# Performance work log

Hardware: AMD Instinct MI355X
Metric: run time of the kernel (lower is better)

## Reference

```python
import jax, jax.numpy as jnp
import numpy as np

NUM_HEADS = 16
LN_EPS = 1e-5


def pos_encoding(length, d):
    pos = jnp.arange(length, dtype=jnp.float32)[:, None]
    i = jnp.arange(d, dtype=jnp.float32)[None, :]
    angle = pos / jnp.power(10000.0, (2.0 * jnp.floor(i / 2.0)) / d)
    return jnp.where((jnp.arange(d) % 2) == 0, jnp.sin(angle), jnp.cos(angle))


def rel_shift(x):
    # x: (B, H, l, m) -> TXL shift trick
    b, h, l, m = x.shape
    x = jnp.concatenate([x, jnp.zeros((b, h, l, 1), x.dtype)], axis=-1)
    x = x.reshape(b, h, l * (m + 1))
    return x[:, :, l - 1:-1].reshape(b, h, l, m)


def layer_norm(x, g, b):
    mu = jnp.mean(x, axis=-1, keepdims=True)
    var = jnp.mean(jnp.square(x - mu), axis=-1, keepdims=True)
    return (x - mu) * jax.lax.rsqrt(var + LN_EPS) * g + b


def setup_inputs() -> dict:
    key = jax.random.key(0)
    B, S, M, D, L, V = 2, 1024, 1024, 1024, 4, 32000
    ks = jax.random.split(key, 32)
    s = 0.02
    d = {
        'inputs': jax.random.randint(ks[0], (B, S), 0, V, dtype=jnp.int32),
        'mems': jax.random.normal(ks[1], (L, B, M, D), jnp.float32),
        'emb': jax.random.normal(ks[2], (V, D), jnp.float32) * s,
        'Wq': jax.random.normal(ks[3], (L, D, D), jnp.float32) * s,
        'bq': jnp.zeros((L, D), jnp.float32),
        'Wke': jax.random.normal(ks[4], (L, D, D), jnp.float32) * s,
        'bke': jnp.zeros((L, D), jnp.float32),
        'Wkr': jax.random.normal(ks[5], (L, D, D), jnp.float32) * s,
        'bkr': jnp.zeros((L, D), jnp.float32),
        'Wv': jax.random.normal(ks[6], (L, D, D), jnp.float32) * s,
        'bv': jnp.zeros((L, D), jnp.float32),
        'Wo': jax.random.normal(ks[7], (L, D, D), jnp.float32) * s,
        'bo': jnp.zeros((L, D), jnp.float32),
        'ln1_g': jnp.ones((L, D), jnp.float32),
        'ln1_b': jnp.zeros((L, D), jnp.float32),
        'W1': jax.random.normal(ks[8], (L, D, D), jnp.float32) * s,
        'b1': jnp.zeros((L, D), jnp.float32),
        'W2': jax.random.normal(ks[9], (L, D, D), jnp.float32) * s,
        'b2': jnp.zeros((L, D), jnp.float32),
        'ln2_g': jnp.ones((L, D), jnp.float32),
        'ln2_b': jnp.zeros((L, D), jnp.float32),
        'Wh': jax.random.normal(ks[10], (D, D), jnp.float32) * s,
        'bh': jnp.zeros((D,), jnp.float32),
        'Wf': jax.random.normal(ks[11], (D, V), jnp.float32) * s,
        'bf': jnp.zeros((V,), jnp.float32),
        'next_mem_len': 1024,
    }
    return d


def reference(inputs, mems, emb, Wq, bq, Wke, bke, Wkr, bkr, Wv, bv, Wo, bo,
              ln1_g, ln1_b, W1, b1, W2, b2, ln2_g, ln2_b, Wh, bh, Wf, bf,
              next_mem_len):
    B, S = inputs.shape
    L, _, M, D = mems.shape
    T = M + S
    H = NUM_HEADS
    dh = D // H
    sqrt_dk = jnp.sqrt(jnp.float32(dh))

    rel_enc = pos_encoding(T, D)[::-1]  # (T, D), reversed
    # look-ahead mask: query i may attend key j iff j <= i + M
    mask = (jnp.arange(T)[None, :] > (jnp.arange(S)[:, None] + M)).astype(jnp.float32)
    mask = mask[None, None] * -1e9  # (1,1,S,T)

    x = emb[inputs] * jnp.sqrt(jnp.float32(D))  # (B,S,D)

    for l in range(L):
        x_tilde = jnp.concatenate([mems[l], x], axis=1)  # (B,T,D)
        q = (x @ Wq[l] + bq[l]).reshape(B, S, H, dh).transpose(0, 2, 1, 3)
        k = (x_tilde @ Wke[l] + bke[l]).reshape(B, T, H, dh).transpose(0, 2, 1, 3)
        v = (x_tilde @ Wv[l] + bv[l]).reshape(B, T, H, dh).transpose(0, 2, 1, 3)
        A = jnp.einsum('bhsd,bhtd->bhst', q, k)
        Qr = (rel_enc @ Wkr[l] + bkr[l]).reshape(T, H, dh).transpose(1, 0, 2)  # (H,T,dh)
        B_hat = jnp.einsum('bhsd,htd->bhst', q, Qr)
        score = (A + rel_shift(B_hat)) / sqrt_dk + mask
        attn = jax.nn.softmax(score, axis=-1)
        ctx = jnp.einsum('bhst,bhtd->bhsd', attn, v)
        ctx = ctx.transpose(0, 2, 1, 3).reshape(B, S, D)
        attn_out = ctx @ Wo[l] + bo[l]
        h1 = layer_norm(x + attn_out, ln1_g[l], ln1_b[l])
        ff = jax.nn.gelu(h1 @ W1[l] + b1[l], approximate=False) @ W2[l] + b2[l]
        x = layer_norm(h1 + ff, ln2_g[l], ln2_b[l])

    x = jax.nn.gelu(x @ Wh + bh, approximate=False)
    logits = x @ Wf + bf
    return logits
```

## Files before the change

kernel.cpp:

```cpp
#include <hip/hip_runtime.h>
#include <hip/hip_bf16.h>
#include <math.h>

typedef __attribute__((ext_vector_type(4))) float f32x4;
typedef __attribute__((ext_vector_type(8))) short s16x8;

#define BB 2
#define SS 1024
#define MEM 1024
#define DD 1024
#define LL 4
#define VV 32000
#define TT 2048
#define NH 16
#define DH 64

__device__ __forceinline__ short f2bf(float f) {
    unsigned u = __float_as_uint(f);
    u += 0x7fffu + ((u >> 16) & 1u);
    return (short)(u >> 16);
}

__device__ __forceinline__ float gelu_f(float x) {
    return 0.5f * x * (1.0f + erff(x * 0.70710678118654752f));
}

__device__ __forceinline__ void gll16(const short* g, short* l) {
    __builtin_amdgcn_global_load_lds(
        (__attribute__((address_space(1))) void*)(short*)g,
        (__attribute__((address_space(3))) void*)l, 16, 0, 0);
}

template<int WM, int WN>
__global__ __launch_bounds__(256) void gemm_bf16(
    const short* __restrict__ A, const short* __restrict__ Bt,
    const float* __restrict__ bias, const float* __restrict__ bias2,
    int nsplit, void* __restrict__ Cv, int N, int K, int nby, int act, int obf)
{
    constexpr int BM = WM * 32, BN = WN * 32;
    constexpr int NA = BM / 32, NB = BN / 32;
    __shared__ short a_s[BM * 64];
    __shared__ short b_s[BN * 64];
    const int tid  = threadIdx.x;
    const int lane = tid & 63;
    const int wave = tid >> 6;
    const int wr = wave >> 1, wc = wave & 1;
    const int fr = lane & 15, fg = lane >> 4;

    const int nwg = gridDim.x;
    const int bid = blockIdx.x;
    const int swz = ((nwg & 7) == 0) ? ((bid & 7) * (nwg >> 3) + (bid >> 3)) : bid;
    const size_t m0 = (size_t)(swz % nby) * BM;
    const size_t n0 = (size_t)(swz / nby) * BN;

    const short* gA[NA]; short* lA[NA];
    const short* gB[NB]; short* lB[NB];
    #pragma unroll
    for (int i = 0; i < NA; ++i) {
        const int s   = i * 256 + tid;
        const int row = (s >> 7) * 16 + (s & 15);
        const int kof = ((s >> 4) & 7) * 8;
        gA[i] = A + (m0 + row) * (size_t)K + kof;
        lA[i] = &a_s[s * 8];
    }
    #pragma unroll
    for (int i = 0; i < NB; ++i) {
        const int s   = i * 256 + tid;
        const int nn  = (s >> 7) * 16 + (s & 15);
        const int kof = ((s >> 4) & 7) * 8;
        gB[i] = Bt + (n0 + nn) * (size_t)K + kof;
        lB[i] = &b_s[s * 8];
    }

    f32x4 acc[WM][WN] = {};

    #pragma unroll
    for (int i = 0; i < NA; ++i) gll16(gA[i], lA[i]);
    #pragma unroll
    for (int i = 0; i < NB; ++i) gll16(gB[i], lB[i]);

    const int nt = K >> 6;
    for (int t = 0; t < nt; ++t) {
        __syncthreads();
        s16x8 af[WM][2], bf[WN][2];
        #pragma unroll
        for (int mi = 0; mi < WM; ++mi)
            #pragma unroll
            for (int h = 0; h < 2; ++h)
                af[mi][h] = *(const s16x8*)&a_s[((wr*WM + mi)*128 + (h*4 + fg)*16 + fr) * 8];
        #pragma unroll
        for (int ni = 0; ni < WN; ++ni)
            #pragma unroll
            for (int h = 0; h < 2; ++h)
                bf[ni][h] = *(const s16x8*)&b_s[((wc*WN + ni)*128 + (h*4 + fg)*16 + fr) * 8];
        if (t + 1 < nt) {
            __syncthreads();
            const int koff = (t + 1) << 6;
            #pragma unroll
            for (int i = 0; i < NA; ++i) gll16(gA[i] + koff, lA[i]);
            #pragma unroll
            for (int i = 0; i < NB; ++i) gll16(gB[i] + koff, lB[i]);
        }
        #pragma unroll
        for (int mi = 0; mi < WM; ++mi)
            #pragma unroll
            for (int ni = 0; ni < WN; ++ni) {
                acc[mi][ni] = __builtin_amdgcn_mfma_f32_16x16x32_bf16(
                    af[mi][0], bf[ni][0], acc[mi][ni], 0, 0, 0);
                acc[mi][ni] = __builtin_amdgcn_mfma_f32_16x16x32_bf16(
                    af[mi][1], bf[ni][1], acc[mi][ni], 0, 0, 0);
            }
    }

    float* Cf = (float*)Cv;
    short* Cb = (short*)Cv;
    #pragma unroll
    for (int mi = 0; mi < WM; ++mi) {
        #pragma unroll
        for (int ni = 0; ni < WN; ++ni) {
            const size_t r0 = m0 + wr*WM*16 + mi*16 + fg*4;
            const size_t c  = n0 + wc*WN*16 + ni*16 + fr;
            const float bb = (c < (size_t)nsplit) ? bias[c] : bias2[c - nsplit];
            #pragma unroll
            for (int rg = 0; rg < 4; ++rg) {
                float vv = acc[mi][ni][rg] + bb;
                if (act) vv = gelu_f(vv);
                if (obf) Cb[(r0 + rg)*(size_t)N + c] = f2bf(vv);
                else     Cf[(r0 + rg)*(size_t)N + c] = vv;
            }
        }
    }
}

__global__ __launch_bounds__(256) void transpose7_kernel(
    const float* w0, const float* w1, const float* w2, const float* w3,
    const float* w4, const float* w5, const float* w6, short* out)
{
    __shared__ float t[32][33];
    const int z = blockIdx.z;
    const float* W;
    switch (z) {
        case 0: W = w0; break; case 1: W = w1; break; case 2: W = w2; break;
        case 3: W = w3; break; case 4: W = w4; break; case 5: W = w5; break;
        default: W = w6; break;
    }
    short* O = out + (size_t)z * DD * DD;
    const int tid = threadIdx.x;
    const int k0 = blockIdx.y * 32, n0 = blockIdx.x * 32;
    const int r = tid >> 3, c4 = (tid & 7) * 4;
    float4 v = *(const float4*)&W[(size_t)(k0 + r) * DD + n0 + c4];
    t[r][c4+0] = v.x; t[r][c4+1] = v.y; t[r][c4+2] = v.z; t[r][c4+3] = v.w;
    __syncthreads();
    short4 o;
    o.x = f2bf(t[c4+0][r]); o.y = f2bf(t[c4+1][r]);
    o.z = f2bf(t[c4+2][r]); o.w = f2bf(t[c4+3][r]);
    *(short4*)&O[(size_t)(n0 + r) * DD + k0 + c4] = o;
}

__global__ __launch_bounds__(256) void transposeF_kernel(
    const float* __restrict__ W, short* __restrict__ O)
{
    __shared__ float t[32][33];
    const int tid = threadIdx.x;
    const int k0 = blockIdx.y * 32, n0 = blockIdx.x * 32;
    const int r = tid >> 3, c4 = (tid & 7) * 4;
    float4 v = *(const float4*)&W[(size_t)(k0 + r) * VV + n0 + c4];
    t[r][c4+0] = v.x; t[r][c4+1] = v.y; t[r][c4+2] = v.z; t[r][c4+3] = v.w;
    __syncthreads();
    short4 o;
    o.x = f2bf(t[c4+0][r]); o.y = f2bf(t[c4+1][r]);
    o.z = f2bf(t[c4+2][r]); o.w = f2bf(t[c4+3][r]);
    *(short4*)&O[(size_t)(n0 + r) * DD + k0 + c4] = o;
}

__global__ __launch_bounds__(256) void attn_kernel(
    const short* __restrict__ q, const short* __restrict__ k,
    const short* __restrict__ v, const short* __restrict__ Qr,
    short* __restrict__ ctx, int kstr, int qstr)
{
    __shared__ short k_s[32][72];
    __shared__ short qr_s[96][72];
    __shared__ short vT_s[64][40];
    __shared__ float a_t[64][33];
    __shared__ float b_ts[64][33];
    __shared__ short p_s[64][40];
    __shared__ float row_m[64], row_l[64], row_sc[64];

    const int tid  = threadIdx.x;
    const int id   = blockIdx.x;
    const int bh   = id & 31;
    const int qi   = ((id >> 5) + bh) & 15;
    const int q0   = qi * 64;
    const int b    = bh >> 4;
    const int h    = bh & 15;
    const int hoff = h * DH;

    const int lane = tid & 63;
    const int wave = tid >> 6;
    const int fr   = lane & 15;
    const int fg   = lane >> 4;
    const int tk  = tid >> 3, ck = (tid & 7) * 8;
    const int iq  = tid >> 2, cq = (tid & 3) * 16;
    const int iq2 = 64 + (tid >> 3), cq2 = (tid & 7) * 8;
    const int sr  = tid >> 2, sc0 = (tid & 3) * 8;

    const short* qrow = q + ((size_t)(b * SS + q0 + 16 * wave + fr)) * DD + hoff;
    s16x8 aq0 = *(const s16x8*)(qrow + fg * 8);
    s16x8 aq1 = *(const s16x8*)(qrow + 32 + fg * 8);

    if (tid < 64) { row_m[tid] = -INFINITY; row_l[tid] = 0.0f; }

    const int t_end = q0 + 64 + MEM;
    const int u0b   = SS - 1 - (q0 + 63);

    s16x8 kf, vf, rA, rB, rC;
    auto loadT = [&](int t0) {
        kf = *(const s16x8*)(k + ((size_t)(b * TT + t0 + tk)) * kstr + hoff + ck);
        vf = *(const s16x8*)(v + ((size_t)(b * TT + t0 + tk)) * kstr + hoff + ck);
        int u1 = t0 + u0b + iq;
        u1 = u1 < 0 ? 0 : (u1 > TT - 1 ? TT - 1 : u1);
        const short* rp = Qr + (size_t)u1 * qstr + hoff + cq;
        rA = *(const s16x8*)rp;
        rB = *(const s16x8*)(rp + 8);
        int u2 = t0 + u0b + iq2;
        u2 = u2 < 0 ? 0 : (u2 > TT - 1 ? TT - 1 : u2);
        rC = *(const s16x8*)(Qr + (size_t)u2 * qstr + hoff + cq2);
    };
    loadT(0);

    f32x4 opv[4] = {};
    const int nlo = 3 - wave, nhi = 5 - wave;

    for (int t0 = 0; t0 < t_end; t0 += 32) {
        __syncthreads();
        {
            *(s16x8*)&k_s[tk][ck] = kf;
            const int tsw = tk ^ (((ck >> 3) & 3) << 3);
            vT_s[ck + 0][tsw] = vf[0];
            vT_s[ck + 1][tsw] = vf[1];
            vT_s[ck + 2][tsw] = vf[2];
            vT_s[ck + 3][tsw] = vf[3];
            vT_s[ck + 4][tsw] = vf[4];
            vT_s[ck + 5][tsw] = vf[5];
            vT_s[ck + 6][tsw] = vf[6];
            vT_s[ck + 7][tsw] = vf[7];
            *(s16x8*)&qr_s[iq][cq]      = rA;
            *(s16x8*)&qr_s[iq][cq + 8]  = rB;
            *(s16x8*)&qr_s[iq2][cq2]    = rC;
        }
        if (t0 + 32 < t_end) loadT(t0 + 32);
        __syncthreads();

        {
            #pragma unroll
            for (int n = 0; n < 2; ++n) {
                s16x8 b0 = *(const s16x8*)&k_s[16*n + fr][fg * 8];
                s16x8 b1 = *(const s16x8*)&k_s[16*n + fr][32 + fg * 8];
                f32x4 ca = {0, 0, 0, 0};
                ca = __builtin_amdgcn_mfma_f32_16x16x32_bf16(aq0, b0, ca, 0, 0, 0);
                ca = __builtin_amdgcn_mfma_f32_16x16x32_bf16(aq1, b1, ca, 0, 0, 0);
                #pragma unroll
                for (int rg = 0; rg < 4; ++rg)
                    a_t[16*wave + 4*fg + rg][16*n + fr] = ca[rg];
            }
        }
        {
            #pragma unroll
            for (int n = 0; n < 6; ++n) {
                if (n < nlo || n > nhi) continue;
                s16x8 c0 = *(const s16x8*)&qr_s[16*n + fr][fg * 8];
                s16x8 c1 = *(const s16x8*)&qr_s[16*n + fr][32 + fg * 8];
                f32x4 cb = {0, 0, 0, 0};
                cb = __builtin_amdgcn_mfma_f32_16x16x32_bf16(aq0, c0, cb, 0, 0, 0);
                cb = __builtin_amdgcn_mfma_f32_16x16x32_bf16(aq1, c1, cb, 0, 0, 0);
                #pragma unroll
                for (int rg = 0; rg < 4; ++rg) {
                    const int r  = 16*wave + 4*fg + rg;
                    const int tl = 16*n + fr - 63 + r;
                    if ((unsigned)tl < 32u) b_ts[r][tl] = cb[rg];
                }
            }
        }
        __syncthreads();

        {
            const int sg = q0 + sr;
            float sv[8];
            #pragma unroll
            for (int j = 0; j < 8; ++j) {
                const int c = sc0 + j;
                float x = (a_t[sr][c] + b_ts[sr][c]) * 0.125f;
                sv[j] = (t0 + c > sg + MEM) ? -1e30f : x;
            }
            float mx = sv[0];
            #pragma unroll
            for (int j = 1; j < 8; ++j) mx = fmaxf(mx, sv[j]);
            mx = fmaxf(mx, __shfl_xor(mx, 1, 64));
            mx = fmaxf(mx, __shfl_xor(mx, 2, 64));
            const float mo = row_m[sr];
            const float mn = fmaxf(mo, mx);
            const float scl = __expf(mo - mn);
            float sum = 0.0f;
            s16x8 pp;
            #pragma unroll
            for (int j = 0; j < 8; ++j) {
                float e = __expf(sv[j] - mn);
                sum += e;
                pp[j] = f2bf(e);
            }
            sum += __shfl_xor(sum, 1, 64);
            sum += __shfl_xor(sum, 2, 64);
            if ((tid & 3) == 0) {
                row_m[sr]  = mn;
                row_sc[sr] = scl;
                row_l[sr]  = row_l[sr] * scl + sum;
            }
            *(s16x8*)&p_s[sr][sc0] = pp;
        }
        __syncthreads();

        {
            f32x4 scv;
            #pragma unroll
            for (int rg = 0; rg < 4; ++rg) scv[rg] = row_sc[16*wave + 4*fg + rg];
            #pragma unroll
            for (int n = 0; n < 4; ++n)
                #pragma unroll
                for (int rg = 0; rg < 4; ++rg) opv[n][rg] *= scv[rg];
            s16x8 ap = *(const s16x8*)&p_s[16*wave + fr][fg * 8];
            #pragma unroll
            for (int n = 0; n < 4; ++n) {
                const int d = 16*n + fr;
                s16x8 bv = *(const s16x8*)&vT_s[d][(fg ^ ((d >> 3) & 3)) * 8];
                opv[n] = __builtin_amdgcn_mfma_f32_16x16x32_bf16(ap, bv, opv[n], 0, 0, 0);
            }
        }
    }

    {
        #pragma unroll
        for (int rg = 0; rg < 4; ++rg) {
            const int r = 16*wave + 4*fg + rg;
            const float inv = 1.0f / row_l[r];
            short* op = ctx + ((size_t)(b * SS + q0 + r)) * DD + hoff;
            #pragma unroll
            for (int n = 0; n < 4; ++n)
                op[16*n + fr] = f2bf(opv[n][rg] * inv);
        }
    }
}

__global__ __launch_bounds__(256) void addln_kernel(
    const float* __restrict__ a, const float* __restrict__ b,
    const float* __restrict__ g, const float* __restrict__ be,
    float* __restrict__ out32, short* __restrict__ outbf)
{
    __shared__ float red[8];
    const int row = blockIdx.x;
    const int tid = threadIdx.x;
    const size_t base = (size_t)row * DD;
    const int c = tid * 4;
    float4 xa = *(const float4*)(a + base + c);
    float4 xb = *(const float4*)(b + base + c);
    float x0 = xa.x + xb.x, x1 = xa.y + xb.y, x2 = xa.z + xb.z, x3 = xa.w + xb.w;
    float s  = x0 + x1 + x2 + x3;
    float sq = x0 * x0 + x1 * x1 + x2 * x2 + x3 * x3;
    #pragma unroll
    for (int o = 32; o > 0; o >>= 1) {
        s  += __shfl_down(s, o, 64);
        sq += __shfl_down(sq, o, 64);
    }
    const int wv = tid >> 6;
    if ((tid & 63) == 0) { red[wv * 2] = s; red[wv * 2 + 1] = sq; }
    __syncthreads();
    float ts = red[0] + red[2] + red[4] + red[6];
    float tq = red[1] + red[3] + red[5] + red[7];
    float mu  = ts * (1.0f / DD);
    float var = tq * (1.0f / DD) - mu * mu;
    float rs  = rsqrtf(var + 1e-5f);
    float4 gv = *(const float4*)(g + c);
    float4 bv = *(const float4*)(be + c);
    float4 o4;
    o4.x = (x0 - mu) * rs * gv.x + bv.x;
    o4.y = (x1 - mu) * rs * gv.y + bv.y;
    o4.z = (x2 - mu) * rs * gv.z + bv.z;
    o4.w = (x3 - mu) * rs * gv.w + bv.w;
    *(float4*)(out32 + base + c) = o4;
    short4 ob;
    ob.x = f2bf(o4.x); ob.y = f2bf(o4.y); ob.z = f2bf(o4.z); ob.w = f2bf(o4.w);
    *(short4*)(outbf + base + c) = ob;
}

__global__ __launch_bounds__(256) void embed_kernel(
    const int* __restrict__ inp, const float* __restrict__ emb,
    float* __restrict__ x32, short* __restrict__ xbf)
{
    const int row = blockIdx.x;
    const int c = threadIdx.x * 4;
    const int idx = inp[row];
    float4 vv = *(const float4*)(emb + (size_t)idx * DD + c);
    vv.x *= 32.0f; vv.y *= 32.0f; vv.z *= 32.0f; vv.w *= 32.0f;
    *(float4*)(x32 + (size_t)row * DD + c) = vv;
    short4 ob;
    ob.x = f2bf(vv.x); ob.y = f2bf(vv.y); ob.z = f2bf(vv.z); ob.w = f2bf(vv.w);
    *(short4*)(xbf + (size_t)row * DD + c) = ob;
}

__global__ __launch_bounds__(256) void concat_kernel(
    const float* __restrict__ mems_l, const short* __restrict__ xbf,
    short* __restrict__ xt)
{
    size_t i = ((size_t)blockIdx.x * 256 + threadIdx.x) * 8;
    size_t bt = i / DD;
    int d = (int)(i - bt * DD);
    int b = (int)(bt / TT);
    int t = (int)(bt - (size_t)b * TT);
    s16x8 o;
    if (t < MEM) {
        const float* mp = mems_l + ((size_t)(b * MEM + t)) * DD + d;
        float4 a0 = *(const float4*)mp;
        float4 a1 = *(const float4*)(mp + 4);
        o[0] = f2bf(a0.x); o[1] = f2bf(a0.y); o[2] = f2bf(a0.z); o[3] = f2bf(a0.w);
        o[4] = f2bf(a1.x); o[5] = f2bf(a1.y); o[6] = f2bf(a1.z); o[7] = f2bf(a1.w);
    } else {
        o = *(const s16x8*)(xbf + ((size_t)(b * SS + (t - MEM))) * DD + d);
    }
    *(s16x8*)(xt + i) = o;
}

__global__ __launch_bounds__(256) void relenc_kernel(short* __restrict__ re)
{
    const int u = blockIdx.x;
    const int p = TT - 1 - u;
    const int i0 = threadIdx.x * 4;
    short4 o;
    #pragma unroll
    for (int j = 0; j < 4; ++j) {
        int i = i0 + j;
        float ex   = (float)(2 * (i >> 1)) * (1.0f / DD);
        float invf = __expf(-ex * 9.210340371976184f);
        float ang  = (float)p * invf;
        float val  = (i & 1) ? cosf(ang) : sinf(ang);
        ((short*)&o)[j] = f2bf(val);
    }
    *(short4*)&re[(size_t)u * DD + i0] = o;
}

extern "C" void kernel_launch(void* const* d_in, const int* in_sizes, int n_in,
                              void* d_out, int out_size, void* d_ws, size_t ws_size,
                              hipStream_t stream)
{
    const int*   inp  = (const int*)d_in[0];
    const float* mems = (const float*)d_in[1];
    const float* emb  = (const float*)d_in[2];
    const float* Wq   = (const float*)d_in[3];
    const float* bq   = (const float*)d_in[4];
    const float* Wke  = (const float*)d_in[5];
    const float* bke  = (const float*)d_in[6];
    const float* Wkr  = (const float*)d_in[7];
    const float* bkr  = (const float*)d_in[8];
    const float* Wv   = (const float*)d_in[9];
    const float* bv   = (const float*)d_in[10];
    const float* Wo   = (const float*)d_in[11];
    const float* bo   = (const float*)d_in[12];
    const float* ln1g = (const float*)d_in[13];
    const float* ln1b = (const float*)d_in[14];
    const float* W1   = (const float*)d_in[15];
    const float* b1   = (const float*)d_in[16];
    const float* W2   = (const float*)d_in[17];
    const float* b2   = (const float*)d_in[18];
    const float* ln2g = (const float*)d_in[19];
    const float* ln2b = (const float*)d_in[20];
    const float* Wh   = (const float*)d_in[21];
    const float* bh   = (const float*)d_in[22];
    const float* Wf   = (const float*)d_in[23];
    const float* bfb  = (const float*)d_in[24];

    char* wsb = (char*)d_ws;
    size_t off = 0;
    auto alloc = [&](size_t bytes) { char* p = wsb + off; off += (bytes + 255) & ~(size_t)255; return p; };
    float* h132  = (float*)alloc((size_t)BB*SS*DD*4);
    float* ao32  = (float*)alloc((size_t)BB*SS*DD*4);
    float* ff232 = (float*)alloc((size_t)BB*SS*DD*4);
    short* xt    = (short*)alloc((size_t)BB*TT*DD*2);
    short* qb    = (short*)alloc((size_t)BB*SS*DD*2);
    short* kvb   = (short*)alloc((size_t)BB*TT*DD*2*2);
    short* ctxb  = (short*)alloc((size_t)BB*SS*DD*2);
    short* ff1   = (short*)alloc((size_t)BB*SS*DD*2);
    float* x32   = (float*)alloc((size_t)BB*SS*DD*4);
    short* x_bf  = (short*)alloc((size_t)BB*SS*DD*2);
    short* whout = (short*)alloc((size_t)BB*SS*DD*2);
    short* rel   = (short*)alloc((size_t)TT*DD*2);
    short* qr4   = (short*)alloc((size_t)SS*2*4*DD*2);
    short* wt6   = (short*)alloc((size_t)6*DD*DD*2);
    short* wkr4  = (short*)h132;
    short* wft   = (short*)h132;

    relenc_kernel<<<TT, 256, 0, stream>>>(rel);
    embed_kernel<<<BB * SS, 256, 0, stream>>>(inp, emb, x32, x_bf);

    const size_t WOFF = (size_t)DD * DD;

    transpose7_kernel<<<dim3(32, 32, 4), 256, 0, stream>>>(
        Wkr + 0*WOFF, Wkr + 1*WOFF, Wkr + 2*WOFF, Wkr + 3*WOFF, Wq, Wq, Wq, wkr4);
    gemm_bf16<4,4><<<dim3(512), 256, 0, stream>>>(
        rel, wkr4, bkr, bkr, 4*DD, qr4, 4*DD, DD, TT/128, 0, 1);

    const int gSm = (DD / 64) * ((BB * SS) / 64);
    const int gKV = ((2 * DD) / 128) * ((BB * TT) / 128);

    for (int l = 0; l < LL; ++l) {
        const size_t wo  = (size_t)l * DD * DD;
        const size_t bo_ = (size_t)l * DD;
        transpose7_kernel<<<dim3(32, 32, 6), 256, 0, stream>>>(
            Wq + wo, Wke + wo, Wv + wo, Wo + wo, W1 + wo, W2 + wo, Wq, wt6);
        concat_kernel<<<(BB * TT * DD / 8) / 256, 256, 0, stream>>>(
            mems + (size_t)l * BB * MEM * DD, x_bf, xt);
        gemm_bf16<2,2><<<dim3(gSm), 256, 0, stream>>>(
            x_bf, wt6 + 0*WOFF, bq + bo_, bq + bo_, DD, qb, DD, DD, (BB*SS)/64, 0, 1);
        gemm_bf16<4,4><<<dim3(gKV), 256, 0, stream>>>(
            xt, wt6 + 1*WOFF, bke + bo_, bv + bo_, DD, kvb, 2*DD, DD, (BB*TT)/128, 0, 1);
        attn_kernel<<<dim3((SS / 64) * BB * NH), 256, 0, stream>>>(
            qb, kvb, kvb + DD, qr4 + (size_t)l * DD, ctxb, 2 * DD, 4 * DD);
        gemm_bf16<2,2><<<dim3(gSm), 256, 0, stream>>>(
            ctxb, wt6 + 3*WOFF, bo + bo_, bo + bo_, DD, ao32, DD, DD, (BB*SS)/64, 0, 0);
        addln_kernel<<<BB * SS, 256, 0, stream>>>(x32, ao32, ln1g + bo_, ln1b + bo_, h132, x_bf);
        gemm_bf16<2,2><<<dim3(gSm), 256, 0, stream>>>(
            x_bf, wt6 + 4*WOFF, b1 + bo_, b1 + bo_, DD, ff1, DD, DD, (BB*SS)/64, 1, 1);
        gemm_bf16<2,2><<<dim3(gSm), 256, 0, stream>>>(
            ff1, wt6 + 5*WOFF, b2 + bo_, b2 + bo_, DD, ff232, DD, DD, (BB*SS)/64, 0, 0);
        addln_kernel<<<BB * SS, 256, 0, stream>>>(h132, ff232, ln2g + bo_, ln2b + bo_, x32, x_bf);
    }

    transpose7_kernel<<<dim3(32, 32, 1), 256, 0, stream>>>(
        Wh, Wh, Wh, Wh, Wh, Wh, Wh, wt6);
    transposeF_kernel<<<dim3(VV / 32, DD / 32), 256, 0, stream>>>(Wf, wft);
    gemm_bf16<2,2><<<dim3(gSm), 256, 0, stream>>>(
        x_bf, wt6, bh, bh, DD, whout, DD, DD, (BB*SS)/64, 1, 1);
    gemm_bf16<4,4><<<dim3((VV / 128) * ((BB * SS) / 128)), 256, 0, stream>>>(
        whout, wft, bfb, bfb, VV, (float*)d_out, VV, DD, (BB*SS)/128, 0, 0);
}
```

Before: 1.415 ms.

## Triple-buffer GEMM K-loop and widen attention tile with wave-local softmax

The GEMM kernel moves from a single-buffer 64-wide K step to a three-stage LDS ring of 32-wide K slices. Global-to-LDS loads are issued two stages ahead and guarded by explicit vmcnt waits and raw barriers, which is meant to hide load latency. The attention kernel doubles its key tile to 64 and accumulates the relative-position term directly into the score buffer, dropping one LDS array. Softmax running max and sum move into registers and are shared with shuffles, removing two block-wide barriers per tile. In exchange, LDS use and register pressure go up, and the correctness of the manual waitcnt and barrier ordering becomes harder to verify.

```diff
diff --git a/kernel.cpp b/kernel.cpp
--- a/kernel.cpp
+++ b/kernel.cpp
@@ -31,6 +31,15 @@
         (__attribute__((address_space(3))) void*)l, 16, 0, 0);
 }
 
+template<int N> __device__ __forceinline__ void vm_wait() {
+    if constexpr (N == 0)      asm volatile("s_waitcnt vmcnt(0)" ::: "memory");
+    else if constexpr (N == 2) asm volatile("s_waitcnt vmcnt(2)" ::: "memory");
+    else if constexpr (N == 3) asm volatile("s_waitcnt vmcnt(3)" ::: "memory");
+    else if constexpr (N == 4) asm volatile("s_waitcnt vmcnt(4)" ::: "memory");
+    else if constexpr (N == 6) asm volatile("s_waitcnt vmcnt(6)" ::: "memory");
+    else                       asm volatile("s_waitcnt vmcnt(8)" ::: "memory");
+}
+
 template<int WM, int WN>
 __global__ __launch_bounds__(256) void gemm_bf16(
     const short* __restrict__ A, const short* __restrict__ Bt,
@@ -38,9 +47,11 @@
     int nsplit, void* __restrict__ Cv, int N, int K, int nby, int act, int obf)
 {
     constexpr int BM = WM * 32, BN = WN * 32;
-    constexpr int NA = BM / 32, NB = BN / 32;
-    __shared__ short a_s[BM * 64];
-    __shared__ short b_s[BN * 64];
+    constexpr int NA = BM / 64, NB = BN / 64;
+    constexpr int L  = NA + NB;
+    constexpr int ASZ = BM * 32, BSZ = BN * 32;
+    __shared__ short a_s[3 * ASZ];
+    __shared__ short b_s[3 * BSZ];
     const int tid  = threadIdx.x;
     const int lane = tid & 63;
     const int wave = tid >> 6;
@@ -58,58 +69,58 @@
     #pragma unroll
     for (int i = 0; i < NA; ++i) {
         const int s   = i * 256 + tid;
-        const int row = (s >> 7) * 16 + (s & 15);
-        const int kof = ((s >> 4) & 7) * 8;
-        gA[i] = A + (m0 + row) * (size_t)K + kof;
+        const int row = (s >> 6) * 16 + (s & 15);
+        const int ks  = (s >> 4) & 3;
+        gA[i] = A + (m0 + row) * (size_t)K + ks * 8;
         lA[i] = &a_s[s * 8];
     }
     #pragma unroll
     for (int i = 0; i < NB; ++i) {
         const int s   = i * 256 + tid;
-        const int nn  = (s >> 7) * 16 + (s & 15);
-        const int kof = ((s >> 4) & 7) * 8;
-        gB[i] = Bt + (n0 + nn) * (size_t)K + kof;
+        const int nn  = (s >> 6) * 16 + (s & 15);
+        const int ks  = (s >> 4) & 3;
+        gB[i] = Bt + (n0 + nn) * (size_t)K + ks * 8;
         lB[i] = &b_s[s * 8];
     }
 
+    auto stage = [&](int t, int buf) {
+        const int koff = t << 5;
+        #pragma unroll
+        for (int i = 0; i < NA; ++i) gll16(gA[i] + koff, lA[i] + buf * ASZ);
+        #pragma unroll
+        for (int i = 0; i < NB; ++i) gll16(gB[i] + koff, lB[i] + buf * BSZ);
+    };
+
     f32x4 acc[WM][WN] = {};
 
-    #pragma unroll
-    for (int i = 0; i < NA; ++i) gll16(gA[i], lA[i]);
-    #pragma unroll
-    for (int i = 0; i < NB; ++i) gll16(gB[i], lB[i]);
-
-    const int nt = K >> 6;
+    const int nt = K >> 5;
+    stage(0, 0);
+    stage(1, 1);
+
+    int cur = 0;
     for (int t = 0; t < nt; ++t) {
-        __syncthreads();
-        s16x8 af[WM][2], bf[WN][2];
+        if (t + 1 < nt) vm_wait<L>();
+        else            vm_wait<0>();
+        __builtin_amdgcn_s_barrier();
+        __builtin_amdgcn_sched_barrier(0);
+        if (t + 2 < nt) stage(t + 2, cur == 0 ? 2 : cur - 1);
+
+        const short* ab = &a_s[cur * ASZ];
+        const short* bb = &b_s[cur * BSZ];
+        s16x8 af[WM], bf[WN];
         #pragma unroll
         for (int mi = 0; mi < WM; ++mi)
-            #pragma unroll
-            for (int h = 0; h < 2; ++h)
-                af[mi][h] = *(const s16x8*)&a_s[((wr*WM + mi)*128 + (h*4 + fg)*16 + fr) * 8];
+            af[mi] = *(const s16x8*)&ab[((wr*WM + mi)*64 + fg*16 + fr) * 8];
         #pragma unroll
         for (int ni = 0; ni < WN; ++ni)
-            #pragma unroll
-            for (int h = 0; h < 2; ++h)
-                bf[ni][h] = *(const s16x8*)&b_s[((wc*WN + ni)*128 + (h*4 + fg)*16 + fr) * 8];
-        if (t + 1 < nt) {
-            __syncthreads();
-            const int koff = (t + 1) << 6;
-            #pragma unroll
-            for (int i = 0; i < NA; ++i) gll16(gA[i] + koff, lA[i]);
-            #pragma unroll
-            for (int i = 0; i < NB; ++i) gll16(gB[i] + koff, lB[i]);
-        }
+            bf[ni] = *(const s16x8*)&bb[((wc*WN + ni)*64 + fg*16 + fr) * 8];
         #pragma unroll
         for (int mi = 0; mi < WM; ++mi)
             #pragma unroll
-            for (int ni = 0; ni < WN; ++ni) {
+            for (int ni = 0; ni < WN; ++ni)
                 acc[mi][ni] = __builtin_amdgcn_mfma_f32_16x16x32_bf16(
-                    af[mi][0], bf[ni][0], acc[mi][ni], 0, 0, 0);
-                acc[mi][ni] = __builtin_amdgcn_mfma_f32_16x16x32_bf16(
-                    af[mi][1], bf[ni][1], acc[mi][ni], 0, 0, 0);
-            }
+                    af[mi], bf[ni], acc[mi][ni], 0, 0, 0);
+        cur = (cur == 2) ? 0 : cur + 1;
     }
 
     float* Cf = (float*)Cv;
@@ -178,13 +189,11 @@
     const short* __restrict__ v, const short* __restrict__ Qr,
     short* __restrict__ ctx, int kstr, int qstr)
 {
-    __shared__ short k_s[32][72];
-    __shared__ short qr_s[96][72];
-    __shared__ short vT_s[64][40];
-    __shared__ float a_t[64][33];
-    __shared__ float b_ts[64][33];
-    __shared__ short p_s[64][40];
-    __shared__ float row_m[64], row_l[64], row_sc[64];
+    __shared__ short k_s[64][72];
+    __shared__ short vT_s[64][72];
+    __shared__ short qr_s[128][72];
+    __shared__ float a_t[64][67];
+    __shared__ short p_s[64][72];
 
     const int tid  = threadIdx.x;
     const int id   = blockIdx.x;
@@ -199,61 +208,63 @@
     const int wave = tid >> 6;
     const int fr   = lane & 15;
     const int fg   = lane >> 4;
-    const int tk  = tid >> 3, ck = (tid & 7) * 8;
-    const int iq  = tid >> 2, cq = (tid & 3) * 16;
-    const int iq2 = 64 + (tid >> 3), cq2 = (tid & 7) * 8;
-    const int sr  = tid >> 2, sc0 = (tid & 3) * 8;
+    const int tk = tid >> 2, ck = (tid & 3) * 16;
+    const int rq = tid >> 1, dq = (tid & 1) * 32;
+    const int sr  = tid >> 2;
+    const int sc0 = (tid & 3) * 16;
 
     const short* qrow = q + ((size_t)(b * SS + q0 + 16 * wave + fr)) * DD + hoff;
     s16x8 aq0 = *(const s16x8*)(qrow + fg * 8);
     s16x8 aq1 = *(const s16x8*)(qrow + 32 + fg * 8);
 
-    if (tid < 64) { row_m[tid] = -INFINITY; row_l[tid] = 0.0f; }
+    float m_r = -1e30f, l_r = 0.0f;
 
     const int t_end = q0 + 64 + MEM;
-    const int u0b   = SS - 1 - (q0 + 63);
-
-    s16x8 kf, vf, rA, rB, rC;
+    const int u0b   = SS - 1 - q0 - 63;
+
+    s16x8 kf0, kf1, vf0, vf1, rf0, rf1, rf2, rf3;
     auto loadT = [&](int t0) {
-        kf = *(const s16x8*)(k + ((size_t)(b * TT + t0 + tk)) * kstr + hoff + ck);
-        vf = *(const s16x8*)(v + ((size_t)(b * TT + t0 + tk)) * kstr + hoff + ck);
-        int u1 = t0 + u0b + iq;
-        u1 = u1 < 0 ? 0 : (u1 > TT - 1 ? TT - 1 : u1);
-        const short* rp = Qr + (size_t)u1 * qstr + hoff + cq;
-        rA = *(const s16x8*)rp;
-        rB = *(const s16x8*)(rp + 8);
-        int u2 = t0 + u0b + iq2;
-        u2 = u2 < 0 ? 0 : (u2 > TT - 1 ? TT - 1 : u2);
-        rC = *(const s16x8*)(Qr + (size_t)u2 * qstr + hoff + cq2);
+        const short* kp = k + ((size_t)(b * TT + t0 + tk)) * kstr + hoff + ck;
+        const short* vp = v + ((size_t)(b * TT + t0 + tk)) * kstr + hoff + ck;
+        kf0 = *(const s16x8*)kp;  kf1 = *(const s16x8*)(kp + 8);
+        vf0 = *(const s16x8*)vp;  vf1 = *(const s16x8*)(vp + 8);
+        int u = t0 + u0b + rq;
+        u = u < 0 ? 0 : (u > TT - 1 ? TT - 1 : u);
+        const short* rp = Qr + (size_t)u * qstr + hoff + dq;
+        rf0 = *(const s16x8*)rp;        rf1 = *(const s16x8*)(rp + 8);
+        rf2 = *(const s16x8*)(rp + 16); rf3 = *(const s16x8*)(rp + 24);
     };
     loadT(0);
 
     f32x4 opv[4] = {};
-    const int nlo = 3 - wave, nhi = 5 - wave;
-
-    for (int t0 = 0; t0 < t_end; t0 += 32) {
-        __syncthreads();
+    const int nlo = 3 - wave, nhi = 7 - wave;
+
+    for (int t0 = 0; t0 < t_end; t0 += 64) {
+        asm volatile("" ::: "memory");
+        __builtin_amdgcn_s_barrier();
+        __builtin_amdgcn_sched_barrier(0);
         {
-            *(s16x8*)&k_s[tk][ck] = kf;
-            const int tsw = tk ^ (((ck >> 3) & 3) << 3);
-            vT_s[ck + 0][tsw] = vf[0];
-            vT_s[ck + 1][tsw] = vf[1];
-            vT_s[ck + 2][tsw] = vf[2];
-            vT_s[ck + 3][tsw] = vf[3];
-            vT_s[ck + 4][tsw] = vf[4];
-            vT_s[ck + 5][tsw] = vf[5];
-            vT_s[ck + 6][tsw] = vf[6];
-            vT_s[ck + 7][tsw] = vf[7];
-            *(s16x8*)&qr_s[iq][cq]      = rA;
-            *(s16x8*)&qr_s[iq][cq + 8]  = rB;
-            *(s16x8*)&qr_s[iq2][cq2]    = rC;
+            *(s16x8*)&k_s[tk][ck]     = kf0;
+            *(s16x8*)&k_s[tk][ck + 8] = kf1;
+            #pragma unroll
+            for (int i = 0; i < 8; ++i) {
+                const int d0 = ck + i, d1 = ck + 8 + i;
+                vT_s[d0][tk ^ (((d0 >> 3) & 3) << 3)] = vf0[i];
+                vT_s[d1][tk ^ (((d1 >> 3) & 3) << 3)] = vf1[i];
+            }
+            *(s16x8*)&qr_s[rq][dq]      = rf0;
+            *(s16x8*)&qr_s[rq][dq + 8]  = rf1;
+            *(s16x8*)&qr_s[rq][dq + 16] = rf2;
+            *(s16x8*)&qr_s[rq][dq + 24] = rf3;
         }
-        if (t0 + 32 < t_end) loadT(t0 + 32);
-        __syncthreads();
+        if (t0 + 64 < t_end) loadT(t0 + 64);
+        asm volatile("s_waitcnt lgkmcnt(0)" ::: "memory");
+        __builtin_amdgcn_s_barrier();
+        __builtin_amdgcn_sched_barrier(0);
 
         {
             #pragma unroll
-            for (int n = 0; n < 2; ++n) {
+            for (int n = 0; n < 4; ++n) {
                 s16x8 b0 = *(const s16x8*)&k_s[16*n + fr][fg * 8];
                 s16x8 b1 = *(const s16x8*)&k_s[16*n + fr][32 + fg * 8];
                 f32x4 ca = {0, 0, 0, 0};
@@ -266,7 +277,7 @@
         }
         {
             #pragma unroll
-            for (int n = 0; n < 6; ++n) {
+            for (int n = 0; n < 8; ++n) {
                 if (n < nlo || n > nhi) continue;
                 s16x8 c0 = *(const s16x8*)&qr_s[16*n + fr][fg * 8];
                 s16x8 c1 = *(const s16x8*)&qr_s[16*n + fr][32 + fg * 8];
@@ -277,71 +288,71 @@
                 for (int rg = 0; rg < 4; ++rg) {
                     const int r  = 16*wave + 4*fg + rg;
                     const int tl = 16*n + fr - 63 + r;
-                    if ((unsigned)tl < 32u) b_ts[r][tl] = cb[rg];
+                    if ((unsigned)tl < 64u) a_t[r][tl] += cb[rg];
                 }
             }
         }
-        __syncthreads();
 
         {
             const int sg = q0 + sr;
-            float sv[8];
-            #pragma unroll
-            for (int j = 0; j < 8; ++j) {
+            float e[16];
+            float mx = -1e30f;
+            #pragma unroll
+            for (int j = 0; j < 16; ++j) {
                 const int c = sc0 + j;
-                float x = (a_t[sr][c] + b_ts[sr][c]) * 0.125f;
-                sv[j] = (t0 + c > sg + MEM) ? -1e30f : x;
-            }
-            float mx = sv[0];
-            #pragma unroll
-            for (int j = 1; j < 8; ++j) mx = fmaxf(mx, sv[j]);
+                float x = a_t[sr][c] * 0.125f;
+                x = (t0 + c > sg + MEM) ? -1e30f : x;
+                e[j] = x;
+                mx = fmaxf(mx, x);
+            }
             mx = fmaxf(mx, __shfl_xor(mx, 1, 64));
             mx = fmaxf(mx, __shfl_xor(mx, 2, 64));
-            const float mo = row_m[sr];
-            const float mn = fmaxf(mo, mx);
-            const float scl = __expf(mo - mn);
+            const float mn  = fmaxf(m_r, mx);
+            const float scl = __expf(m_r - mn);
             float sum = 0.0f;
-            s16x8 pp;
-            #pragma unroll
-            for (int j = 0; j < 8; ++j) {
-                float e = __expf(sv[j] - mn);
-                sum += e;
-                pp[j] = f2bf(e);
+            s16x8 p0, p1;
+            #pragma unroll
+            for (int j = 0; j < 16; ++j) {
+                float ev = __expf(e[j] - mn);
+                sum += ev;
+                if (j < 8) p0[j] = f2bf(ev); else p1[j - 8] = f2bf(ev);
             }
             sum += __shfl_xor(sum, 1, 64);
             sum += __shfl_xor(sum, 2, 64);
-            if ((tid & 3) == 0) {
-                row_m[sr]  = mn;
-                row_sc[sr] = scl;
-                row_l[sr]  = row_l[sr] * scl + sum;
-            }
-            *(s16x8*)&p_s[sr][sc0] = pp;
-        }
-        __syncthreads();
-
-        {
+            l_r = l_r * scl + sum;
+            m_r = mn;
+            *(s16x8*)&p_s[sr][sc0]     = p0;
+            *(s16x8*)&p_s[sr][sc0 + 8] = p1;
+
             f32x4 scv;
             #pragma unroll
-            for (int rg = 0; rg < 4; ++rg) scv[rg] = row_sc[16*wave + 4*fg + rg];
+            for (int rg = 0; rg < 4; ++rg) scv[rg] = __shfl(scl, 16*fg + 4*rg, 64);
             #pragma unroll
             for (int n = 0; n < 4; ++n)
                 #pragma unroll
                 for (int rg = 0; rg < 4; ++rg) opv[n][rg] *= scv[rg];
-            s16x8 ap = *(const s16x8*)&p_s[16*wave + fr][fg * 8];
+            s16x8 ap0 = *(const s16x8*)&p_s[16*wave + fr][fg * 8];
+            s16x8 ap1 = *(const s16x8*)&p_s[16*wave + fr][32 + fg * 8];
             #pragma unroll
             for (int n = 0; n < 4; ++n) {
-                const int d = 16*n + fr;
-                s16x8 bv = *(const s16x8*)&vT_s[d][(fg ^ ((d >> 3) & 3)) * 8];
-                opv[n] = __builtin_amdgcn_mfma_f32_16x16x32_bf16(ap, bv, opv[n], 0, 0, 0);
+                const int d  = 16*n + fr;
+                const int xw = (d >> 3) & 3;
+                s16x8 bv0 = *(const s16x8*)&vT_s[d][(fg ^ xw) * 8];
+                s16x8 bv1 = *(const s16x8*)&vT_s[d][32 + (fg ^ xw) * 8];
+                opv[n] = __builtin_amdgcn_mfma_f32_16x16x32_bf16(ap0, bv0, opv[n], 0, 0, 0);
+                opv[n] = __builtin_amdgcn_mfma_f32_16x16x32_bf16(ap1, bv1, opv[n], 0, 0, 0);
             }
         }
     }
 
     {
+        f32x4 lv;
+        #pragma unroll
+        for (int rg = 0; rg < 4; ++rg) lv[rg] = __shfl(l_r, 16*fg + 4*rg, 64);
         #pragma unroll
         for (int rg = 0; rg < 4; ++rg) {
             const int r = 16*wave + 4*fg + rg;
-            const float inv = 1.0f / row_l[r];
+            const float inv = 1.0f / lv[rg];
             short* op = ctx + ((size_t)(b * SS + q0 + r)) * DD + hoff;
             #pragma unroll
             for (int n = 0; n < 4; ++n)
```

Result: slower. 1.451 ms (+2.5%).
